# Performance work log

Measured on AMD Instinct MI355X. Metric: run time of the kernel, lower is better.

Reference implementation:

```python
import jax, jax.numpy as jnp
import numpy as np

MAX_DISP = 4          # init kwarg
WIN = 2 * MAX_DISP + 1  # 9 -> 81 displacement offsets
CHUNK = 16            # hardcoded channel chunk size in the torch module


def setup_inputs() -> dict:
    key = jax.random.key(0)
    k1, k2 = jax.random.split(key)
    B, C, H, W = 8, 128, 96, 160
    x1 = jax.random.normal(k1, (B, C, H, W), dtype=jnp.float32)
    x2 = jax.random.normal(k2, (B, C, H, W), dtype=jnp.float32)
    return {"x1": x1, "x2": x2}


def reference(x1, x2):
    B, C, H, W = x2.shape
    pad = MAX_DISP
    # replicate padding == torch F.pad mode='replicate' == jnp 'edge'
    x2p = jnp.pad(x2, ((0, 0), (0, 0), (pad, pad), (pad, pad)), mode="edge")
    # offsets in the same row-major (dy outer, dx inner) order as the torch loops
    dy, dx = jnp.meshgrid(jnp.arange(-pad, pad + 1), jnp.arange(-pad, pad + 1), indexing="ij")
    offsets = jnp.stack([dy.ravel(), dx.ravel()], axis=1)  # [81, 2]
    num_chunks = -(-C // CHUNK)  # ceil(C/16); with C%16==0 chunk-mean == total-sum/num_chunks

    def body(carry, off):
        # shifted window of x2: x2p[:, :, pad+dy : pad+dy+H, pad+dx : pad+dx+W]
        sl = jax.lax.dynamic_slice(x2p, (0, 0, pad + off[0], pad + off[1]), (B, C, H, W))
        return carry, jnp.sum(x1 * sl, axis=1)  # [B, H, W]

    _, corr = jax.lax.scan(body, None, offsets)  # [81, B, H, W]
    corr = jnp.transpose(corr, (1, 0, 2, 3))     # [B, 81, H, W]
    return corr / jnp.asarray(num_chunks, corr.dtype)
```

## Files before the change

kernel.cpp:

```cpp
#include <hip/hip_runtime.h>
#include <cstdint>

#define BB 8
#define CC 128
#define HH 96
#define WW 160
#define HWsz (HH * WW)
#define TH 8
#define TW 32
#define CSTEP 8
#define HALO_H (TH + 8)
#define HALO_W (TW + 8)
#define CH_WORDS (HALO_H * HALO_W)
#define CHUNK_WORDS (CSTEP * CH_WORDS)
#define NWAVES 9
#define NTHREADS (NWAVES * 64)
#define WLOADS (CHUNK_WORDS / 64)
#define NCHUNKS (CC / CSTEP)
#define NBLOCKS (BB * (HH / TH) * (WW / TW))

__device__ __forceinline__ void g2l_dword(const float* g, float* l) {
  __builtin_amdgcn_global_load_lds((const __attribute__((address_space(1))) void*)g,
                                   (__attribute__((address_space(3))) void*)l,
                                   4, 0, 0);
}

extern "C" __global__ void __launch_bounds__(NTHREADS, 2)
corr81_kernel(const float* __restrict__ x1, const float* __restrict__ x2,
              float* __restrict__ out)
{
  __shared__ __align__(16) float lds[2][CHUNK_WORDS];

  const int tid  = threadIdx.x;
  const int wv   = tid >> 6;
  const int lane = tid & 63;
  const int r    = lane >> 3;
  const int j    = lane & 7;

  const int bid = blockIdx.x;
  const int wt  = bid % (WW / TW);
  const int ht  = (bid / (WW / TW)) % (HH / TH);
  const int b   = bid / ((WW / TW) * (HH / TH));
  const int h0  = ht * TH;
  const int w0  = wt * TW;

  uint32_t soff[9];
#pragma unroll
  for (int i = 0; i < 9; ++i) {
    const int idx = wv + 9 * i;
    const int e   = idx * 64 + lane;
    const int ci  = e / CH_WORDS;
    const int rem = e - ci * CH_WORDS;
    const int hr  = rem / HALO_W;
    const int wh  = rem - hr * HALO_W;
    int gh = h0 + hr - 4; gh = gh < 0 ? 0 : (gh > HH - 1 ? HH - 1 : gh);
    int gw = w0 + wh - 4; gw = gw < 0 ? 0 : (gw > WW - 1 ? WW - 1 : gw);
    soff[i] = (uint32_t)((ci * HH + gh) * WW + gw);
  }

  const float* x2b = x2 + (size_t)b * CC * HWsz;
  const float* x1b = x1 + (size_t)b * CC * HWsz + (size_t)(h0 + r) * WW + (w0 + 4 * j);

  float acc[9][4];
#pragma unroll
  for (int dx = 0; dx < 9; ++dx)
#pragma unroll
    for (int p = 0; p < 4; ++p) acc[dx][p] = 0.f;

  const int rowbase = (r + wv) * HALO_W + 4 * j;

  {
    const float* src = x2b;
#pragma unroll
    for (int i = 0; i < 9; ++i) {
      const int idx = wv + 9 * i;
      if (idx < WLOADS)
        g2l_dword(src + soff[i], &lds[0][idx * 64]);
    }
  }
  __syncthreads();

#pragma unroll 1
  for (int chunk = 0; chunk < NCHUNKS; ++chunk) {
    const int cb = chunk & 1;
    const int sb = cb ^ 1;

    if (chunk + 1 < NCHUNKS) {
      const float* src = x2b + (size_t)(chunk + 1) * (CSTEP * HWsz);
#pragma unroll
      for (int i = 0; i < 9; ++i) {
        const int idx = wv + 9 * i;
        if (idx < WLOADS)
          g2l_dword(src + soff[i], &lds[sb][idx * 64]);
      }
    }

#pragma unroll
    for (int ci = 0; ci < CSTEP; ++ci) {
      const float4 a4 = *(const float4*)(x1b + (size_t)(chunk * CSTEP + ci) * HWsz);
      const float av[4] = {a4.x, a4.y, a4.z, a4.w};
      const float4* wr = (const float4*)&lds[cb][ci * CH_WORDS + rowbase];
      const float4 f0 = wr[0];
      const float4 f1 = wr[1];
      const float4 f2 = wr[2];
      const float w12[12] = {f0.x, f0.y, f0.z, f0.w,
                             f1.x, f1.y, f1.z, f1.w,
                             f2.x, f2.y, f2.z, f2.w};
#pragma unroll
      for (int dx = 0; dx < 9; ++dx)
#pragma unroll
        for (int p = 0; p < 4; ++p)
          acc[dx][p] = fmaf(av[p], w12[dx + p], acc[dx][p]);
    }

    __syncthreads();
  }

  float* op = out + (((size_t)b * 81 + (size_t)wv * 9) * HH + (h0 + r)) * WW + (w0 + 4 * j);
#pragma unroll
  for (int dx = 0; dx < 9; ++dx) {
    float4 v;
    v.x = acc[dx][0] * 0.125f;
    v.y = acc[dx][1] * 0.125f;
    v.z = acc[dx][2] * 0.125f;
    v.w = acc[dx][3] * 0.125f;
    *(float4*)(op + (size_t)dx * HWsz) = v;
  }
}

extern "C" void kernel_launch(void* const* d_in, const int* in_sizes, int n_in,
                              void* d_out, int out_size, void* d_ws, size_t ws_size,
                              hipStream_t stream) {
  const float* x1 = (const float*)d_in[0];
  const float* x2 = (const float*)d_in[1];
  float* out = (float*)d_out;
  corr81_kernel<<<dim3(NBLOCKS), dim3(NTHREADS), 0, stream>>>(x1, x2, out);
}
```

Before: 212.6 us.

## Widen per-thread register tile, split channels across half-waves, swizzle LDS rows

Each thread now computes 8 output columns for 9 dx offsets and handles half of each channel chunk, so LDS reads (four float4 per channel) are reused over 72 FMAs instead of 36. The two half-wave partial sums are combined with a cross-lane shuffle before the store. The LDS staging is rewritten as per-row 48-word loads into a 64-word stride with an XOR swizzle to reduce bank conflicts. Block IDs are remapped, and launch bounds are raised to 5, which targets higher occupancy but risks register pressure from the 72 accumulators.

```diff
diff --git a/kernel.cpp b/kernel.cpp
--- a/kernel.cpp
+++ b/kernel.cpp
@@ -9,13 +9,13 @@
 #define TH 8
 #define TW 32
 #define CSTEP 8
-#define HALO_H (TH + 8)
-#define HALO_W (TW + 8)
-#define CH_WORDS (HALO_H * HALO_W)
-#define CHUNK_WORDS (CSTEP * CH_WORDS)
+#define HALO_H 16
+#define SW 64
+#define CI_WORDS (HALO_H * SW)
+#define BUF_WORDS (CSTEP * CI_WORDS)
 #define NWAVES 9
 #define NTHREADS (NWAVES * 64)
-#define WLOADS (CHUNK_WORDS / 64)
+#define NSLOTS (CSTEP * HALO_H)
 #define NCHUNKS (CC / CSTEP)
 #define NBLOCKS (BB * (HH / TH) * (WW / TW))
 
@@ -25,106 +25,112 @@
                                    4, 0, 0);
 }
 
-extern "C" __global__ void __launch_bounds__(NTHREADS, 2)
+__device__ __forceinline__ void stage_chunk(const float* __restrict__ src, float* dst,
+                                            int h0, int w0, int lane, int wvu) {
+  for (int slot = wvu; slot < NSLOTS; slot += NWAVES) {
+    const int ci  = slot >> 4;
+    const int row = slot & 15;
+    int gh = h0 + row - 4; gh = gh < 0 ? 0 : (gh > HH - 1 ? HH - 1 : gh);
+    const int cl = lane ^ ((row & 3) << 2);
+    int gw = w0 + cl - 4; gw = gw < 0 ? 0 : (gw > WW - 1 ? WW - 1 : gw);
+    if (lane < 48)
+      g2l_dword(src + (ci * HH + gh) * WW + gw, dst + ci * CI_WORDS + row * SW);
+  }
+}
+
+extern "C" __global__ void __launch_bounds__(NTHREADS, 5)
 corr81_kernel(const float* __restrict__ x1, const float* __restrict__ x2,
               float* __restrict__ out)
 {
-  __shared__ __align__(16) float lds[2][CHUNK_WORDS];
+  __shared__ __align__(16) float lds[2][BUF_WORDS];
 
   const int tid  = threadIdx.x;
   const int wv   = tid >> 6;
+  const int wvu  = __builtin_amdgcn_readfirstlane(wv);
   const int lane = tid & 63;
-  const int r    = lane >> 3;
-  const int j    = lane & 7;
+  const int h    = lane >> 5;
+  const int r    = (lane >> 2) & 7;
+  const int s    = lane & 3;
 
-  const int bid = blockIdx.x;
-  const int wt  = bid % (WW / TW);
-  const int ht  = (bid / (WW / TW)) % (HH / TH);
-  const int b   = bid / ((WW / TW) * (HH / TH));
-  const int h0  = ht * TH;
-  const int w0  = wt * TW;
+  const int bid0 = blockIdx.x;
+  const int bid  = (bid0 & 7) * (NBLOCKS / 8) + (bid0 >> 3);
 
-  uint32_t soff[9];
+  const int wt = bid % (WW / TW);
+  const int ht = (bid / (WW / TW)) % (HH / TH);
+  const int b  = bid / ((WW / TW) * (HH / TH));
+  const int h0 = ht * TH;
+  const int w0 = wt * TW;
+
+  const int R  = r + wv;
+  const int fx = (R & 3) << 2;
+  int A[4];
 #pragma unroll
-  for (int i = 0; i < 9; ++i) {
-    const int idx = wv + 9 * i;
-    const int e   = idx * 64 + lane;
-    const int ci  = e / CH_WORDS;
-    const int rem = e - ci * CH_WORDS;
-    const int hr  = rem / HALO_W;
-    const int wh  = rem - hr * HALO_W;
-    int gh = h0 + hr - 4; gh = gh < 0 ? 0 : (gh > HH - 1 ? HH - 1 : gh);
-    int gw = w0 + wh - 4; gw = gw < 0 ? 0 : (gw > WW - 1 ? WW - 1 : gw);
-    soff[i] = (uint32_t)((ci * HH + gh) * WW + gw);
-  }
+  for (int t = 0; t < 4; ++t)
+    A[t] = h * 4096 + R * SW + ((8 * s + 4 * t) ^ fx);
 
   const float* x2b = x2 + (size_t)b * CC * HWsz;
-  const float* x1b = x1 + (size_t)b * CC * HWsz + (size_t)(h0 + r) * WW + (w0 + 4 * j);
+  const float* x1p = x1 + ((size_t)b * CC + 4 * h) * HWsz
+                        + (size_t)(h0 + r) * WW + (w0 + 8 * s);
 
-  float acc[9][4];
+  float acc[9][8];
 #pragma unroll
-  for (int dx = 0; dx < 9; ++dx)
+  for (int d = 0; d < 9; ++d)
 #pragma unroll
-    for (int p = 0; p < 4; ++p) acc[dx][p] = 0.f;
+    for (int p = 0; p < 8; ++p) acc[d][p] = 0.f;
 
-  const int rowbase = (r + wv) * HALO_W + 4 * j;
-
-  {
-    const float* src = x2b;
-#pragma unroll
-    for (int i = 0; i < 9; ++i) {
-      const int idx = wv + 9 * i;
-      if (idx < WLOADS)
-        g2l_dword(src + soff[i], &lds[0][idx * 64]);
-    }
-  }
+  stage_chunk(x2b, &lds[0][0], h0, w0, lane, wvu);
   __syncthreads();
 
 #pragma unroll 1
   for (int chunk = 0; chunk < NCHUNKS; ++chunk) {
-    const int cb = chunk & 1;
-    const int sb = cb ^ 1;
+    if (chunk + 1 < NCHUNKS)
+      stage_chunk(x2b + (size_t)(chunk + 1) * (CSTEP * HWsz),
+                  &lds[(chunk + 1) & 1][0], h0, w0, lane, wvu);
 
-    if (chunk + 1 < NCHUNKS) {
-      const float* src = x2b + (size_t)(chunk + 1) * (CSTEP * HWsz);
+    const float* lb = &lds[0][0];
 #pragma unroll
-      for (int i = 0; i < 9; ++i) {
-        const int idx = wv + 9 * i;
-        if (idx < WLOADS)
-          g2l_dword(src + soff[i], &lds[sb][idx * 64]);
+    for (int q = 0; q < 4; ++q) {
+      const float* x1q = x1p + (size_t)q * HWsz;
+      const float4 a0 = ((const float4*)x1q)[0];
+      const float4 a1 = ((const float4*)x1q)[1];
+      const float av[8] = {a0.x, a0.y, a0.z, a0.w, a1.x, a1.y, a1.z, a1.w};
+      float w16[16];
+#pragma unroll
+      for (int t = 0; t < 4; ++t) {
+        const float4 f = *(const float4*)(lb + A[t] + q * 1024);
+        w16[4*t+0] = f.x; w16[4*t+1] = f.y; w16[4*t+2] = f.z; w16[4*t+3] = f.w;
       }
+#pragma unroll
+      for (int d = 0; d < 9; ++d)
+#pragma unroll
+        for (int p = 0; p < 8; ++p)
+          acc[d][p] = fmaf(av[p], w16[d + p], acc[d][p]);
     }
 
-#pragma unroll
-    for (int ci = 0; ci < CSTEP; ++ci) {
-      const float4 a4 = *(const float4*)(x1b + (size_t)(chunk * CSTEP + ci) * HWsz);
-      const float av[4] = {a4.x, a4.y, a4.z, a4.w};
-      const float4* wr = (const float4*)&lds[cb][ci * CH_WORDS + rowbase];
-      const float4 f0 = wr[0];
-      const float4 f1 = wr[1];
-      const float4 f2 = wr[2];
-      const float w12[12] = {f0.x, f0.y, f0.z, f0.w,
-                             f1.x, f1.y, f1.z, f1.w,
-                             f2.x, f2.y, f2.z, f2.w};
-#pragma unroll
-      for (int dx = 0; dx < 9; ++dx)
-#pragma unroll
-        for (int p = 0; p < 4; ++p)
-          acc[dx][p] = fmaf(av[p], w12[dx + p], acc[dx][p]);
-    }
-
+    x1p += (size_t)CSTEP * HWsz;
+    const int flip = (chunk & 1) ? -BUF_WORDS : BUF_WORDS;
+    A[0] += flip; A[1] += flip; A[2] += flip; A[3] += flip;
     __syncthreads();
   }
 
-  float* op = out + (((size_t)b * 81 + (size_t)wv * 9) * HH + (h0 + r)) * WW + (w0 + 4 * j);
+  float* op = out + (((size_t)b * 81 + (size_t)wv * 9) * HH + (h0 + r)) * WW
+                  + (w0 + 8 * s + 4 * h);
 #pragma unroll
-  for (int dx = 0; dx < 9; ++dx) {
+  for (int d = 0; d < 9; ++d) {
+    const float own0 = h ? acc[d][4] : acc[d][0];
+    const float own1 = h ? acc[d][5] : acc[d][1];
+    const float own2 = h ? acc[d][6] : acc[d][2];
+    const float own3 = h ? acc[d][7] : acc[d][3];
+    const float snd0 = h ? acc[d][0] : acc[d][4];
+    const float snd1 = h ? acc[d][1] : acc[d][5];
+    const float snd2 = h ? acc[d][2] : acc[d][6];
+    const float snd3 = h ? acc[d][3] : acc[d][7];
     float4 v;
-    v.x = acc[dx][0] * 0.125f;
-    v.y = acc[dx][1] * 0.125f;
-    v.z = acc[dx][2] * 0.125f;
-    v.w = acc[dx][3] * 0.125f;
-    *(float4*)(op + (size_t)dx * HWsz) = v;
+    v.x = (own0 + __shfl_xor(snd0, 32)) * 0.125f;
+    v.y = (own1 + __shfl_xor(snd1, 32)) * 0.125f;
+    v.z = (own2 + __shfl_xor(snd2, 32)) * 0.125f;
+    v.w = (own3 + __shfl_xor(snd3, 32)) * 0.125f;
+    *(float4*)(op + (size_t)d * HWsz) = v;
   }
 }
 
```

Result: slower. 487.5 us (+129.3%).

## Stage x1 through LDS with async loads and pipeline using explicit vmcnt waits

Applied to the files above, without the earlier changes.

x1 tiles are now loaded into LDS through global_load_lds alongside the x2 halo, double-buffered. This replaces the per-thread global float4 loads inside the compute loop. The loop waits with an explicit s_waitcnt vmcnt(13) so the next chunk's 13 loads stay in flight during compute, with raw s_barriers and sched_barriers in place of __syncthreads. Block IDs are remapped with an XCD-style swizzle, and load slots are clamped rather than predicated, so some loads are redundant. LDS use grows and correctness now depends on the hand-counted vmcnt.

```diff
diff --git a/kernel.cpp b/kernel.cpp
--- a/kernel.cpp
+++ b/kernel.cpp
@@ -9,15 +9,18 @@
 #define TH 8
 #define TW 32
 #define CSTEP 8
-#define HALO_H (TH + 8)
-#define HALO_W (TW + 8)
+#define HALO_H 16
+#define HALO_W 40
 #define CH_WORDS (HALO_H * HALO_W)
-#define CHUNK_WORDS (CSTEP * CH_WORDS)
+#define X2_WORDS (CSTEP * CH_WORDS)
+#define X1_WORDS (CSTEP * TH * TW)
+#define X2_SLOTS (X2_WORDS / 64)
+#define X1_SLOTS (X1_WORDS / 64)
 #define NWAVES 9
 #define NTHREADS (NWAVES * 64)
-#define WLOADS (CHUNK_WORDS / 64)
 #define NCHUNKS (CC / CSTEP)
 #define NBLOCKS (BB * (HH / TH) * (WW / TW))
+#define X1BASE (2 * X2_WORDS)
 
 __device__ __forceinline__ void g2l_dword(const float* g, float* l) {
   __builtin_amdgcn_global_load_lds((const __attribute__((address_space(1))) void*)g,
@@ -29,25 +32,28 @@
 corr81_kernel(const float* __restrict__ x1, const float* __restrict__ x2,
               float* __restrict__ out)
 {
-  __shared__ __align__(16) float lds[2][CHUNK_WORDS];
+  __shared__ __align__(16) float lds[2 * X2_WORDS + 2 * X1_WORDS];
 
   const int tid  = threadIdx.x;
   const int wv   = tid >> 6;
+  const int wvu  = __builtin_amdgcn_readfirstlane(wv);
   const int lane = tid & 63;
   const int r    = lane >> 3;
   const int j    = lane & 7;
 
-  const int bid = blockIdx.x;
-  const int wt  = bid % (WW / TW);
-  const int ht  = (bid / (WW / TW)) % (HH / TH);
-  const int b   = bid / ((WW / TW) * (HH / TH));
-  const int h0  = ht * TH;
-  const int w0  = wt * TW;
+  const int bid0 = blockIdx.x;
+  const int bid  = (bid0 & 7) * (NBLOCKS / 8) + (bid0 >> 3);
 
-  uint32_t soff[9];
+  const int wt = bid % (WW / TW);
+  const int ht = (bid / (WW / TW)) % (HH / TH);
+  const int b  = bid / ((WW / TW) * (HH / TH));
+  const int h0 = ht * TH;
+  const int w0 = wt * TW;
+
+  uint32_t soff2[9]; uint32_t doff2[9];
 #pragma unroll
   for (int i = 0; i < 9; ++i) {
-    const int idx = wv + 9 * i;
+    int idx = wvu + 9 * i; if (idx >= X2_SLOTS) idx = X2_SLOTS - 1;
     const int e   = idx * 64 + lane;
     const int ci  = e / CH_WORDS;
     const int rem = e - ci * CH_WORDS;
@@ -55,76 +61,121 @@
     const int wh  = rem - hr * HALO_W;
     int gh = h0 + hr - 4; gh = gh < 0 ? 0 : (gh > HH - 1 ? HH - 1 : gh);
     int gw = w0 + wh - 4; gw = gw < 0 ? 0 : (gw > WW - 1 ? WW - 1 : gw);
-    soff[i] = (uint32_t)((ci * HH + gh) * WW + gw);
+    soff2[i] = (uint32_t)((ci * HH + gh) * WW + gw);
+    doff2[i] = (uint32_t)(idx * 64);
+  }
+  uint32_t soff1[4]; uint32_t doff1[4];
+#pragma unroll
+  for (int i = 0; i < 4; ++i) {
+    int idx = wvu + 9 * i; if (idx >= X1_SLOTS) idx = X1_SLOTS - 1;
+    const int e   = idx * 64 + lane;
+    const int ci  = e >> 8;
+    const int rem = e & 255;
+    const int row = rem >> 5;
+    const int col = rem & 31;
+    soff1[i] = (uint32_t)(ci * HWsz + (h0 + row) * WW + (w0 + col));
+    doff1[i] = (uint32_t)(idx * 64);
   }
 
   const float* x2b = x2 + (size_t)b * CC * HWsz;
-  const float* x1b = x1 + (size_t)b * CC * HWsz + (size_t)(h0 + r) * WW + (w0 + 4 * j);
+  const float* x1b = x1 + (size_t)b * CC * HWsz;
 
   float acc[9][4];
 #pragma unroll
-  for (int dx = 0; dx < 9; ++dx)
+  for (int d = 0; d < 9; ++d)
 #pragma unroll
-    for (int p = 0; p < 4; ++p) acc[dx][p] = 0.f;
+    for (int p = 0; p < 4; ++p) acc[d][p] = 0.f;
 
   const int rowbase = (r + wv) * HALO_W + 4 * j;
+  const int abase   = r * TW + 4 * j;
 
-  {
-    const float* src = x2b;
 #pragma unroll
-    for (int i = 0; i < 9; ++i) {
-      const int idx = wv + 9 * i;
-      if (idx < WLOADS)
-        g2l_dword(src + soff[i], &lds[0][idx * 64]);
-    }
-  }
-  __syncthreads();
+  for (int i = 0; i < 9; ++i) g2l_dword(x2b + soff2[i], &lds[doff2[i]]);
+#pragma unroll
+  for (int i = 0; i < 4; ++i) g2l_dword(x1b + soff1[i], &lds[X1BASE + doff1[i]]);
 
 #pragma unroll 1
-  for (int chunk = 0; chunk < NCHUNKS; ++chunk) {
-    const int cb = chunk & 1;
-    const int sb = cb ^ 1;
+  for (int k = 0; k < NCHUNKS - 1; ++k) {
+    {
+      const int nb = (k + 1) & 1;
+      const float* s2 = x2b + (size_t)(k + 1) * (CSTEP * HWsz);
+      const float* s1 = x1b + (size_t)(k + 1) * (CSTEP * HWsz);
+      float* d2 = &lds[nb * X2_WORDS];
+      float* d1 = &lds[X1BASE + nb * X1_WORDS];
+#pragma unroll
+      for (int i = 0; i < 9; ++i) g2l_dword(s2 + soff2[i], d2 + doff2[i]);
+#pragma unroll
+      for (int i = 0; i < 4; ++i) g2l_dword(s1 + soff1[i], d1 + doff1[i]);
+    }
 
-    if (chunk + 1 < NCHUNKS) {
-      const float* src = x2b + (size_t)(chunk + 1) * (CSTEP * HWsz);
+    asm volatile("s_waitcnt vmcnt(13)" ::: "memory");
+    __builtin_amdgcn_sched_barrier(0);
+    __builtin_amdgcn_s_barrier();
+    __builtin_amdgcn_sched_barrier(0);
+
+    {
+      const float* xb = &lds[(k & 1) * X2_WORDS] + rowbase;
+      const float* ab = &lds[X1BASE + (k & 1) * X1_WORDS] + abase;
 #pragma unroll
-      for (int i = 0; i < 9; ++i) {
-        const int idx = wv + 9 * i;
-        if (idx < WLOADS)
-          g2l_dword(src + soff[i], &lds[sb][idx * 64]);
+      for (int ci = 0; ci < CSTEP; ++ci) {
+        const float4 a4 = *(const float4*)(ab + ci * (TH * TW));
+        const float4* wr = (const float4*)(xb + ci * CH_WORDS);
+        const float4 f0 = wr[0];
+        const float4 f1 = wr[1];
+        const float4 f2 = wr[2];
+        const float av[4] = {a4.x, a4.y, a4.z, a4.w};
+        const float w12[12] = {f0.x, f0.y, f0.z, f0.w,
+                               f1.x, f1.y, f1.z, f1.w,
+                               f2.x, f2.y, f2.z, f2.w};
+#pragma unroll
+        for (int d = 0; d < 9; ++d)
+#pragma unroll
+          for (int p = 0; p < 4; ++p)
+            acc[d][p] = fmaf(av[p], w12[d + p], acc[d][p]);
       }
     }
 
+    __builtin_amdgcn_sched_barrier(0);
+    __builtin_amdgcn_s_barrier();
+    __builtin_amdgcn_sched_barrier(0);
+  }
+
+  asm volatile("s_waitcnt vmcnt(0)" ::: "memory");
+  __builtin_amdgcn_sched_barrier(0);
+  __builtin_amdgcn_s_barrier();
+  __builtin_amdgcn_sched_barrier(0);
+  {
+    const int k = NCHUNKS - 1;
+    const float* xb = &lds[(k & 1) * X2_WORDS] + rowbase;
+    const float* ab = &lds[X1BASE + (k & 1) * X1_WORDS] + abase;
 #pragma unroll
     for (int ci = 0; ci < CSTEP; ++ci) {
-      const float4 a4 = *(const float4*)(x1b + (size_t)(chunk * CSTEP + ci) * HWsz);
-      const float av[4] = {a4.x, a4.y, a4.z, a4.w};
-      const float4* wr = (const float4*)&lds[cb][ci * CH_WORDS + rowbase];
+      const float4 a4 = *(const float4*)(ab + ci * (TH * TW));
+      const float4* wr = (const float4*)(xb + ci * CH_WORDS);
       const float4 f0 = wr[0];
       const float4 f1 = wr[1];
       const float4 f2 = wr[2];
+      const float av[4] = {a4.x, a4.y, a4.z, a4.w};
       const float w12[12] = {f0.x, f0.y, f0.z, f0.w,
                              f1.x, f1.y, f1.z, f1.w,
                              f2.x, f2.y, f2.z, f2.w};
 #pragma unroll
-      for (int dx = 0; dx < 9; ++dx)
+      for (int d = 0; d < 9; ++d)
 #pragma unroll
         for (int p = 0; p < 4; ++p)
-          acc[dx][p] = fmaf(av[p], w12[dx + p], acc[dx][p]);
+          acc[d][p] = fmaf(av[p], w12[d + p], acc[d][p]);
     }
-
-    __syncthreads();
   }
 
   float* op = out + (((size_t)b * 81 + (size_t)wv * 9) * HH + (h0 + r)) * WW + (w0 + 4 * j);
 #pragma unroll
-  for (int dx = 0; dx < 9; ++dx) {
+  for (int d = 0; d < 9; ++d) {
     float4 v;
-    v.x = acc[dx][0] * 0.125f;
-    v.y = acc[dx][1] * 0.125f;
-    v.z = acc[dx][2] * 0.125f;
-    v.w = acc[dx][3] * 0.125f;
-    *(float4*)(op + (size_t)dx * HWsz) = v;
+    v.x = acc[d][0] * 0.125f;
+    v.y = acc[d][1] * 0.125f;
+    v.z = acc[d][2] * 0.125f;
+    v.w = acc[d][3] * 0.125f;
+    *(float4*)(op + (size_t)d * HWsz) = v;
   }
 }
 
```

Result: no change. 210.2 us (-1.1%).
